# Optimization experiments

Hardware: AMD Instinct MI355X
Metric: run time of the kernel (lower is better)

## Reference

```python
import jax, jax.numpy as jnp
import numpy as np

EPS_Q = 1e-5
EPS_RMS = 1e-6


def _bitlinear(x, w):
    # absmean ternary weight quantization with STE (STE irrelevant for fwd)
    w_scale = jnp.maximum(jnp.mean(jnp.abs(w)), EPS_Q)
    w_q = jnp.clip(jnp.round(w / w_scale), -1.0, 1.0)
    w_q = jax.lax.stop_gradient(w_q - w) + w
    # per-token absmax activation quantization
    x_scale = jnp.maximum(jnp.max(jnp.abs(x), axis=-1, keepdims=True), EPS_Q)
    x_s = x / x_scale
    out = jnp.einsum('bi,oi->bo', x_s, w_q)
    return out * x_scale


def _rmsnorm(x, g):
    rms = jnp.sqrt(jnp.mean(x * x, axis=-1, keepdims=True) + EPS_RMS)
    return x / rms * g


def setup_inputs() -> dict:
    key = jax.random.key(0)
    ks = jax.random.split(key, 6)
    B, IN, H, OUT = 65536, 784, 1024, 10
    return {
        'x': jax.random.normal(ks[0], (B, IN), dtype=jnp.float32),
        'w1': jax.random.normal(ks[1], (H, IN), dtype=jnp.float32) * 0.02,
        'g1': jnp.ones((H,), dtype=jnp.float32),
        'w2': jax.random.normal(ks[2], (H, H), dtype=jnp.float32) * 0.02,
        'g2': jnp.ones((H,), dtype=jnp.float32),
        'w3': jax.random.normal(ks[3], (OUT, H), dtype=jnp.float32) * 0.02,
    }


def reference(x, w1, g1, w2, g2, w3):
    h = _bitlinear(x, w1)
    h = jax.nn.gelu(_rmsnorm(h, g1), approximate=False)
    h = _bitlinear(h, w2)
    h = jax.nn.gelu(_rmsnorm(h, g2), approximate=False)
    return _bitlinear(h, w3)
```

## Files before the change

### kernel.cpp

```cpp
#include <hip/hip_runtime.h>
#include <hip/hip_bf16.h>
#include <stdint.h>


typedef __attribute__((ext_vector_type(8))) short short8;
typedef __attribute__((ext_vector_type(4))) float f32x4;

#define B_TOTAL 65536
#define IN_DIM 784
#define IN_PAD 896
#define H_DIM 1024
#define OUT_DIM 10
#define OUT_PAD 16

__device__ __forceinline__ unsigned short f2bf(float f) {
    union { float f; unsigned u; } c; c.f = f;
    unsigned r = c.u + 0x7FFFu + ((c.u >> 16) & 1u);
    return (unsigned short)(r >> 16);
}
__device__ __forceinline__ float bf2f(unsigned short h) {
    union { unsigned u; float f; } c; c.u = ((unsigned)h) << 16;
    return c.f;
}

__device__ __forceinline__ float gelu_fast(float t) {
    const float z = t * 0.70710678118f;
    const float s = fabsf(z);
    const float tt = 1.0f / (1.0f + 0.3275911f * s);
    const float e = __expf(-s * s);
    float p = fmaf(tt, 1.061405429f, -1.453152027f);
    p = fmaf(tt, p, 1.421413741f);
    p = fmaf(tt, p, -0.284496736f);
    p = fmaf(tt, p, 0.254829592f);
    float erfa = fmaf(-p * tt, e, 1.0f);
    erfa = copysignf(erfa, z);
    return 0.5f * t * (1.0f + erfa);
}

#define GLOAD16(gp, lp)                                                        \
    __builtin_amdgcn_global_load_lds(                                          \
        (const __attribute__((address_space(1))) void*)(gp),                   \
        (__attribute__((address_space(3))) void*)(lp), 16, 0, 0)

__global__ void absum3_kernel(const float* __restrict__ w1, const float* __restrict__ w2,
                              const float* __restrict__ w3, double* acc) {
    __shared__ float red[4];
    const int which = blockIdx.y;
    const float* w = (which == 0) ? w1 : (which == 1) ? w2 : w3;
    const int n = (which == 0) ? H_DIM * IN_DIM : (which == 1) ? H_DIM * H_DIM : OUT_DIM * H_DIM;
    float s = 0.f;
    for (int i = blockIdx.x * blockDim.x + threadIdx.x; i < n; i += gridDim.x * blockDim.x)
        s += fabsf(w[i]);
#pragma unroll
    for (int o = 32; o > 0; o >>= 1) s += __shfl_xor(s, o);
    if ((threadIdx.x & 63) == 0) red[threadIdx.x >> 6] = s;
    __syncthreads();
    if (threadIdx.x == 0) {
        float t = red[0] + red[1] + red[2] + red[3];
        atomicAdd(acc + which, (double)t);
    }
}

__global__ void quant_all(const float* __restrict__ w1, const float* __restrict__ w2,
                          const float* __restrict__ w3,
                          unsigned short* __restrict__ w1q, unsigned short* __restrict__ w2q,
                          unsigned short* __restrict__ w3q, const double* sums) {
    const int k = blockIdx.x * blockDim.x + threadIdx.x;
    const int y = blockIdx.y;
    const float* w; unsigned short* wq; int o, O, K, Kp, n; const double* sum;
    if (y < 1024)      { w = w1; wq = w1q; o = y;        O = H_DIM;  K = IN_DIM; Kp = IN_PAD; n = H_DIM * IN_DIM;  sum = sums + 0; }
    else if (y < 2048) { w = w2; wq = w2q; o = y - 1024; O = H_DIM;  K = H_DIM;  Kp = H_DIM;  n = H_DIM * H_DIM;  sum = sums + 1; }
    else               { w = w3; wq = w3q; o = y - 2048; O = OUT_DIM; K = H_DIM; Kp = H_DIM;  n = OUT_DIM * H_DIM; sum = sums + 2; }
    if (k >= Kp) return;
    float scale = fmaxf((float)(*sum / (double)n), 1e-5f);
    float q = 0.f;
    if (o < O && k < K) {
        float r = rintf(w[(size_t)o * K + k] / scale);
        q = fminf(1.f, fmaxf(-1.f, r));
    }
    wq[(size_t)o * Kp + k] = f2bf(q);
}

__global__ __launch_bounds__(256)
void convert_pad(const float* __restrict__ x, unsigned short* __restrict__ xb) {
    const int g = blockIdx.x * 256 + threadIdx.x;
    const int row = g / 112;
    const int c = (g % 112) * 8;
    short8 v = 0;
    if (c < IN_DIM) {
        const float* p = x + (size_t)row * IN_DIM + c;
        float4 f0 = *(const float4*)p;
        float4 f1 = *(const float4*)(p + 4);
        v[0] = (short)f2bf(f0.x); v[1] = (short)f2bf(f0.y);
        v[2] = (short)f2bf(f0.z); v[3] = (short)f2bf(f0.w);
        v[4] = (short)f2bf(f1.x); v[5] = (short)f2bf(f1.y);
        v[6] = (short)f2bf(f1.z); v[7] = (short)f2bf(f1.w);
    }
    *(short8*)(xb + (size_t)row * IN_PAD + c) = v;
}

template<int KP>
__global__ __launch_bounds__(512, 2)
void gemm_bt(const unsigned short* __restrict__ A, const unsigned short* __restrict__ Bq,
             unsigned short* __restrict__ C) {
    constexpr int NT = KP / 64;
    __shared__ __attribute__((aligned(16))) unsigned short LDS[65536];
    const int tid = threadIdx.x;
    const int lane = tid & 63;
    const int w = tid >> 6;
    const int wm = w >> 2, wn = w & 3;
    const int lr = lane & 15, gq = lane >> 4;
    const int gsw8 = (gq ^ ((lr >> 3) << 1)) * 8;
    const int lrO = lr * 32;
    const int bid = blockIdx.x;
    const int xcd = bid & 7, slot = bid >> 3;
    const int nblk = slot & 3;
    const int mblk = xcd * (gridDim.x >> 5) + (slot >> 2);
    const int m0 = mblk * 256, n0 = nblk * 256;
    const int rS = lane >> 2;
    const int cS = ((lane & 3) ^ ((lane >> 5) << 1)) * 8;
    const int stA0 = w;
    const int stA1 = 8 + w;
    const int stB_P1 = (w >> 2) * 8 + (w & 3);
    const int stB_P3 = stB_P1 + 4;

#define STG(gbase, areaS, st)                                                  \
    {   const unsigned short* _g = (gbase) +                                   \
            (size_t)(((st) >> 1) * 16 + rS) * KP + ((st) & 1) * 32 + cS;       \
        GLOAD16(_g, &LDS[(areaS) + (st) * 512]);                               \
        GLOAD16(_g + (size_t)128 * KP, &LDS[(areaS) + (st) * 512 + 8192]); }
#define ABASE(t) (A + (size_t)m0 * KP + (t) * 64)
#define BBASE(t) (Bq + (size_t)n0 * KP + (t) * 64)
#define LD_A(mq)                                                               \
    _Pragma("unroll") for (int mf = 0; mf < 4; ++mf)                           \
    _Pragma("unroll") for (int kk = 0; kk < 2; ++kk)                           \
        af[mf][kk] = *(const short8*)&LDS[curS +                               \
            ((wm * 8 + (mq) * 4 + mf) * 2 + kk) * 512 + lrO + gsw8];
#define LD_B(nq)                                                               \
    _Pragma("unroll") for (int nf = 0; nf < 2; ++nf)                           \
    _Pragma("unroll") for (int kk = 0; kk < 2; ++kk)                           \
        bf[nf][kk] = *(const short8*)&LDS[curS + 16384 +                       \
            ((wn * 4 + (nq) * 2 + nf) * 2 + kk) * 512 + lrO + gsw8];
#define QMM(mq, nq)                                                            \
    _Pragma("unroll") for (int kk = 0; kk < 2; ++kk)                           \
    _Pragma("unroll") for (int mf = 0; mf < 4; ++mf)                           \
    _Pragma("unroll") for (int nf = 0; nf < 2; ++nf)                           \
        acc[(mq) * 4 + mf][(nq) * 2 + nf] =                                    \
            __builtin_amdgcn_mfma_f32_16x16x32_bf16(af[mf][kk], bf[nf][kk],    \
                acc[(mq) * 4 + mf][(nq) * 2 + nf], 0, 0, 0);

    f32x4 acc[8][4] = {};
    short8 af[4][2], bf[2][2];
    STG(ABASE(0), 0, stA0);
    STG(BBASE(0), 16384, stB_P1);
    STG(BBASE(0), 16384, stB_P3);
    STG(ABASE(0), 0, stA1);
    STG(ABASE(1), 32768, stA0);
    STG(BBASE(1), 49152, stB_P3);
    STG(ABASE(1), 32768, stA1);
    asm volatile("s_waitcnt vmcnt(6)" ::: "memory");
#pragma unroll 2
    for (int t = 0; t < NT; ++t) {
        const int curS = (t & 1) * 32768;
        const int nxtS = curS ^ 32768;
        __builtin_amdgcn_s_barrier();
        LD_A(0); LD_B(0);
        __builtin_amdgcn_s_setprio(1); QMM(0, 0); __builtin_amdgcn_s_setprio(0);
        if (t + 1 < NT) STG(BBASE(t + 1), nxtS + 16384, stB_P1);
        __builtin_amdgcn_s_barrier();
        LD_B(1);
        __builtin_amdgcn_s_setprio(1); QMM(0, 1); __builtin_amdgcn_s_setprio(0);
        if (t + 2 < NT) STG(ABASE(t + 2), curS, stA0);
        __builtin_amdgcn_s_barrier();
        LD_A(1);
        __builtin_amdgcn_s_setprio(1); QMM(1, 1); __builtin_amdgcn_s_setprio(0);
        if (t + 2 < NT) STG(BBASE(t + 2), curS + 16384, stB_P3);
        __builtin_amdgcn_s_barrier();
        LD_B(0);
        __builtin_amdgcn_s_setprio(1); QMM(1, 0); __builtin_amdgcn_s_setprio(0);
        if (t + 2 < NT) STG(ABASE(t + 2), curS, stA1);
        if (t < NT - 2) {
            asm volatile("s_waitcnt vmcnt(6)" ::: "memory");
        } else {
            asm volatile("s_waitcnt vmcnt(0)" ::: "memory");
        }
    }
#pragma unroll
    for (int mf = 0; mf < 8; ++mf) {
        const int grow = m0 + wm * 128 + mf * 16 + (lane >> 4) * 4;
#pragma unroll
        for (int nf = 0; nf < 4; ++nf) {
            const int gcol = n0 + wn * 64 + nf * 16 + lr;
            unsigned short* Cp = C + (size_t)grow * H_DIM + gcol;
#pragma unroll
            for (int j = 0; j < 4; ++j) Cp[(size_t)j * H_DIM] = f2bf(acc[mf][nf][j]);
        }
    }
#undef STG
#undef ABASE
#undef BBASE
#undef LD_A
#undef LD_B
#undef QMM
}

__global__ __launch_bounds__(256)
void norm_gelu(const unsigned short* __restrict__ Hp, const float* __restrict__ g,
               unsigned short* __restrict__ U) {
    const int row = blockIdx.x * 4 + (threadIdx.x >> 6);
    const int lane = threadIdx.x & 63;
    const unsigned short* rp = Hp + (size_t)row * H_DIM;
    short8 v0 = *(const short8*)(rp + lane * 8);
    short8 v1 = *(const short8*)(rp + 512 + lane * 8);
    float f[16];
#pragma unroll
    for (int j = 0; j < 8; ++j) {
        f[j] = bf2f((unsigned short)v0[j]);
        f[8 + j] = bf2f((unsigned short)v1[j]);
    }
    float s = 0.f;
#pragma unroll
    for (int j = 0; j < 16; ++j) s += f[j] * f[j];
#pragma unroll
    for (int o = 32; o > 0; o >>= 1) s += __shfl_xor(s, o);
    const float rinv = 1.f / sqrtf(s * (1.f / 1024.f) + 1e-6f);
    float4 ga0 = *(const float4*)(g + lane * 8);
    float4 ga1 = *(const float4*)(g + lane * 8 + 4);
    float4 gb0 = *(const float4*)(g + 512 + lane * 8);
    float4 gb1 = *(const float4*)(g + 512 + lane * 8 + 4);
    float gv[16] = {ga0.x, ga0.y, ga0.z, ga0.w, ga1.x, ga1.y, ga1.z, ga1.w,
                    gb0.x, gb0.y, gb0.z, gb0.w, gb1.x, gb1.y, gb1.z, gb1.w};
    short8 o0, o1;
#pragma unroll
    for (int j = 0; j < 8; ++j) {
        o0[j] = (short)f2bf(gelu_fast(f[j] * rinv * gv[j]));
        o1[j] = (short)f2bf(gelu_fast(f[8 + j] * rinv * gv[8 + j]));
    }
    unsigned short* up = U + (size_t)row * H_DIM;
    *(short8*)(up + lane * 8) = o0;
    *(short8*)(up + 512 + lane * 8) = o1;
}

__global__ __launch_bounds__(256)
void norm_gelu_out(const unsigned short* __restrict__ Hp, const float* __restrict__ g,
                   const unsigned short* __restrict__ w3q, float* __restrict__ out) {
    __shared__ unsigned short Us[16][1032];
    __shared__ unsigned short Ws[16][1032];
    const int tid = threadIdx.x;
    const int lane = tid & 63, wid = tid >> 6;
    const size_t r0 = (size_t)blockIdx.x * 16;
    for (int i = tid; i < 2048; i += 256) {
        const int r = i >> 7, cg = i & 127;
        *(short8*)&Ws[r][cg * 8] = *(const short8*)(w3q + (size_t)r * H_DIM + cg * 8);
    }
    float4 ga0 = *(const float4*)(g + lane * 8);
    float4 ga1 = *(const float4*)(g + lane * 8 + 4);
    float4 gb0 = *(const float4*)(g + 512 + lane * 8);
    float4 gb1 = *(const float4*)(g + 512 + lane * 8 + 4);
    float gv[16] = {ga0.x, ga0.y, ga0.z, ga0.w, ga1.x, ga1.y, ga1.z, ga1.w,
                    gb0.x, gb0.y, gb0.z, gb0.w, gb1.x, gb1.y, gb1.z, gb1.w};
#pragma unroll
    for (int rr = 0; rr < 4; ++rr) {
        const int row = wid * 4 + rr;
        const unsigned short* rp = Hp + (r0 + row) * H_DIM;
        short8 v0 = *(const short8*)(rp + lane * 8);
        short8 v1 = *(const short8*)(rp + 512 + lane * 8);
        float f[16];
#pragma unroll
        for (int j = 0; j < 8; ++j) {
            f[j] = bf2f((unsigned short)v0[j]);
            f[8 + j] = bf2f((unsigned short)v1[j]);
        }
        float s = 0.f;
#pragma unroll
        for (int j = 0; j < 16; ++j) s += f[j] * f[j];
#pragma unroll
        for (int o = 32; o > 0; o >>= 1) s += __shfl_xor(s, o);
        const float rinv = 1.f / sqrtf(s * (1.f / 1024.f) + 1e-6f);
        short8 o0, o1;
#pragma unroll
        for (int j = 0; j < 8; ++j) {
            o0[j] = (short)f2bf(gelu_fast(f[j] * rinv * gv[j]));
            o1[j] = (short)f2bf(gelu_fast(f[8 + j] * rinv * gv[8 + j]));
        }
        *(short8*)&Us[row][lane * 8] = o0;
        *(short8*)&Us[row][512 + lane * 8] = o1;
    }
    __syncthreads();
    if (wid == 0) {
        const int lr = lane & 15, lk = (lane >> 4) * 8;
        f32x4 acc = {};
#pragma unroll
        for (int ks = 0; ks < 32; ++ks) {
            short8 a = *(const short8*)&Us[lr][ks * 32 + lk];
            short8 b = *(const short8*)&Ws[lr][ks * 32 + lk];
            acc = __builtin_amdgcn_mfma_f32_16x16x32_bf16(a, b, acc, 0, 0, 0);
        }
        if (lr < OUT_DIM) {
#pragma unroll
            for (int j = 0; j < 4; ++j)
                out[(r0 + (lane >> 4) * 4 + j) * OUT_DIM + lr] = acc[j];
        }
    }
}

extern "C" void kernel_launch(void* const* d_in, const int* in_sizes, int n_in,
                              void* d_out, int out_size, void* d_ws, size_t ws_size,
                              hipStream_t stream) {
    (void)in_sizes; (void)n_in; (void)out_size;
    const float* x  = (const float*)d_in[0];
    const float* w1 = (const float*)d_in[1];
    const float* g1 = (const float*)d_in[2];
    const float* w2 = (const float*)d_in[3];
    const float* g2 = (const float*)d_in[4];
    const float* w3 = (const float*)d_in[5];
    float* out = (float*)d_out;

    uint8_t* ws = (uint8_t*)d_ws;
    double* sums = (double*)ws;
    size_t off = 256;
    unsigned short* w1q = (unsigned short*)(ws + off); off += (size_t)H_DIM * IN_PAD * 2;
    unsigned short* w2q = (unsigned short*)(ws + off); off += (size_t)H_DIM * H_DIM * 2;
    unsigned short* w3q = (unsigned short*)(ws + off); off += (size_t)OUT_PAD * H_DIM * 2;

    size_t rem = (ws_size > off) ? ws_size - off : 0;
    int R = B_TOTAL;
    while (R > 2048 && (size_t)2 * R * H_DIM * 2 > rem) R >>= 1;
    unsigned short* bufA = (unsigned short*)(ws + off);
    unsigned short* bufB = bufA + (size_t)R * H_DIM;

    hipMemsetAsync(sums, 0, 3 * sizeof(double), stream);
    absum3_kernel<<<dim3(128, 3), 256, 0, stream>>>(w1, w2, w3, sums);
    quant_all<<<dim3(4, 2064), 256, 0, stream>>>(w1, w2, w3, w1q, w2q, w3q, sums);

    const int nchunk = B_TOTAL / R;
    for (int c = 0; c < nchunk; ++c) {
        const float* xc = x + (size_t)c * R * IN_DIM;
        convert_pad<<<R * 112 / 256, 256, 0, stream>>>(xc, bufB);
        gemm_bt<IN_PAD><<<(R / 256) * 4, 512, 0, stream>>>(bufB, w1q, bufA);
        norm_gelu<<<R / 4, 256, 0, stream>>>(bufA, g1, bufB);
        gemm_bt<H_DIM><<<(R / 256) * 4, 512, 0, stream>>>(bufB, w2q, bufA);
        norm_gelu_out<<<R / 16, 256, 0, stream>>>(bufA, g2, w3q, out + (size_t)c * R * OUT_DIM);
    }
}
```

Before: 463.1 us.

## Restructure GEMM to 4 waves with 128x128 per-wave tiles and simple double buffer

The bf16 GEMM goes from 8 waves per 512-thread block (each wave computing 128x64) to 4 waves per 256-thread block, each computing a 128x128 sub-tile with 64 accumulators. The four-phase interleaved staging schedule with partial vmcnt waits is replaced by a plain double buffer: load all fragments, issue the next tile's global-to-LDS copies, run the MFMAs, then wait for all loads and barrier. This raises register reuse per wave and cuts barriers, but register pressure rises a lot, only one block per CU fits, and global-load latency is less hidden behind compute.

```diff
diff --git a/kernel.cpp b/kernel.cpp
--- a/kernel.cpp
+++ b/kernel.cpp
@@ -100,7 +100,7 @@
 }
 
 template<int KP>
-__global__ __launch_bounds__(512, 2)
+__global__ __launch_bounds__(256, 1)
 void gemm_bt(const unsigned short* __restrict__ A, const unsigned short* __restrict__ Bq,
              unsigned short* __restrict__ C) {
     constexpr int NT = KP / 64;
@@ -108,7 +108,7 @@
     const int tid = threadIdx.x;
     const int lane = tid & 63;
     const int w = tid >> 6;
-    const int wm = w >> 2, wn = w & 3;
+    const int wm = w >> 1, wn = w & 1;
     const int lr = lane & 15, gq = lane >> 4;
     const int gsw8 = (gq ^ ((lr >> 3) << 1)) * 8;
     const int lrO = lr * 32;
@@ -119,89 +119,64 @@
     const int m0 = mblk * 256, n0 = nblk * 256;
     const int rS = lane >> 2;
     const int cS = ((lane & 3) ^ ((lane >> 5) << 1)) * 8;
-    const int stA0 = w;
-    const int stA1 = 8 + w;
-    const int stB_P1 = (w >> 2) * 8 + (w & 3);
-    const int stB_P3 = stB_P1 + 4;
-
-#define STG(gbase, areaS, st)                                                  \
-    {   const unsigned short* _g = (gbase) +                                   \
-            (size_t)(((st) >> 1) * 16 + rS) * KP + ((st) & 1) * 32 + cS;       \
-        GLOAD16(_g, &LDS[(areaS) + (st) * 512]);                               \
-        GLOAD16(_g + (size_t)128 * KP, &LDS[(areaS) + (st) * 512 + 8192]); }
-#define ABASE(t) (A + (size_t)m0 * KP + (t) * 64)
-#define BBASE(t) (Bq + (size_t)n0 * KP + (t) * 64)
-#define LD_A(mq)                                                               \
-    _Pragma("unroll") for (int mf = 0; mf < 4; ++mf)                           \
-    _Pragma("unroll") for (int kk = 0; kk < 2; ++kk)                           \
-        af[mf][kk] = *(const short8*)&LDS[curS +                               \
-            ((wm * 8 + (mq) * 4 + mf) * 2 + kk) * 512 + lrO + gsw8];
-#define LD_B(nq)                                                               \
-    _Pragma("unroll") for (int nf = 0; nf < 2; ++nf)                           \
-    _Pragma("unroll") for (int kk = 0; kk < 2; ++kk)                           \
-        bf[nf][kk] = *(const short8*)&LDS[curS + 16384 +                       \
-            ((wn * 4 + (nq) * 2 + nf) * 2 + kk) * 512 + lrO + gsw8];
-#define QMM(mq, nq)                                                            \
-    _Pragma("unroll") for (int kk = 0; kk < 2; ++kk)                           \
-    _Pragma("unroll") for (int mf = 0; mf < 4; ++mf)                           \
-    _Pragma("unroll") for (int nf = 0; nf < 2; ++nf)                           \
-        acc[(mq) * 4 + mf][(nq) * 2 + nf] =                                    \
-            __builtin_amdgcn_mfma_f32_16x16x32_bf16(af[mf][kk], bf[nf][kk],    \
-                acc[(mq) * 4 + mf][(nq) * 2 + nf], 0, 0, 0);
-
-    f32x4 acc[8][4] = {};
-    short8 af[4][2], bf[2][2];
-    STG(ABASE(0), 0, stA0);
-    STG(BBASE(0), 16384, stB_P1);
-    STG(BBASE(0), 16384, stB_P3);
-    STG(ABASE(0), 0, stA1);
-    STG(ABASE(1), 32768, stA0);
-    STG(BBASE(1), 49152, stB_P3);
-    STG(ABASE(1), 32768, stA1);
-    asm volatile("s_waitcnt vmcnt(6)" ::: "memory");
+
+#define STAGE_TILE(t, bufS)                                                    \
+    _Pragma("unroll") for (int i = 0; i < 8; ++i) {                            \
+        const int st = w * 8 + i;                                              \
+        const int srow = (st >> 1) * 16 + rS;                                  \
+        const int scol = (t) * 64 + (st & 1) * 32 + cS;                        \
+        GLOAD16(A + (size_t)(m0 + srow) * KP + scol, &LDS[(bufS) + st * 512]); \
+        GLOAD16(Bq + (size_t)(n0 + srow) * KP + scol,                          \
+                &LDS[(bufS) + 16384 + st * 512]);                              \
+    }
+
+    f32x4 acc[8][8] = {};
+    short8 af[8][2], bf[8][2];
+    STAGE_TILE(0, 0);
+    asm volatile("s_waitcnt vmcnt(0)" ::: "memory");
+    __builtin_amdgcn_s_barrier();
 #pragma unroll 2
     for (int t = 0; t < NT; ++t) {
-        const int curS = (t & 1) * 32768;
-        const int nxtS = curS ^ 32768;
+        const int bufS = (t & 1) * 32768;
+        const int nxtS = bufS ^ 32768;
+#pragma unroll
+        for (int mf = 0; mf < 8; ++mf)
+            af[mf][0] = *(const short8*)&LDS[bufS + ((wm * 8 + mf) * 2 + 0) * 512 + lrO + gsw8];
+#pragma unroll
+        for (int nf = 0; nf < 8; ++nf)
+            bf[nf][0] = *(const short8*)&LDS[bufS + 16384 + ((wn * 8 + nf) * 2 + 0) * 512 + lrO + gsw8];
+#pragma unroll
+        for (int mf = 0; mf < 8; ++mf)
+            af[mf][1] = *(const short8*)&LDS[bufS + ((wm * 8 + mf) * 2 + 1) * 512 + lrO + gsw8];
+#pragma unroll
+        for (int nf = 0; nf < 8; ++nf)
+            bf[nf][1] = *(const short8*)&LDS[bufS + 16384 + ((wn * 8 + nf) * 2 + 1) * 512 + lrO + gsw8];
+        if (t + 1 < NT) STAGE_TILE(t + 1, nxtS);
+        __builtin_amdgcn_s_setprio(1);
+#pragma unroll
+        for (int kk = 0; kk < 2; ++kk)
+#pragma unroll
+            for (int mf = 0; mf < 8; ++mf)
+#pragma unroll
+                for (int nf = 0; nf < 8; ++nf)
+                    acc[mf][nf] = __builtin_amdgcn_mfma_f32_16x16x32_bf16(
+                        af[mf][kk], bf[nf][kk], acc[mf][nf], 0, 0, 0);
+        __builtin_amdgcn_s_setprio(0);
+        asm volatile("s_waitcnt vmcnt(0)" ::: "memory");
         __builtin_amdgcn_s_barrier();
-        LD_A(0); LD_B(0);
-        __builtin_amdgcn_s_setprio(1); QMM(0, 0); __builtin_amdgcn_s_setprio(0);
-        if (t + 1 < NT) STG(BBASE(t + 1), nxtS + 16384, stB_P1);
-        __builtin_amdgcn_s_barrier();
-        LD_B(1);
-        __builtin_amdgcn_s_setprio(1); QMM(0, 1); __builtin_amdgcn_s_setprio(0);
-        if (t + 2 < NT) STG(ABASE(t + 2), curS, stA0);
-        __builtin_amdgcn_s_barrier();
-        LD_A(1);
-        __builtin_amdgcn_s_setprio(1); QMM(1, 1); __builtin_amdgcn_s_setprio(0);
-        if (t + 2 < NT) STG(BBASE(t + 2), curS + 16384, stB_P3);
-        __builtin_amdgcn_s_barrier();
-        LD_B(0);
-        __builtin_amdgcn_s_setprio(1); QMM(1, 0); __builtin_amdgcn_s_setprio(0);
-        if (t + 2 < NT) STG(ABASE(t + 2), curS, stA1);
-        if (t < NT - 2) {
-            asm volatile("s_waitcnt vmcnt(6)" ::: "memory");
-        } else {
-            asm volatile("s_waitcnt vmcnt(0)" ::: "memory");
-        }
     }
 #pragma unroll
     for (int mf = 0; mf < 8; ++mf) {
         const int grow = m0 + wm * 128 + mf * 16 + (lane >> 4) * 4;
 #pragma unroll
-        for (int nf = 0; nf < 4; ++nf) {
-            const int gcol = n0 + wn * 64 + nf * 16 + lr;
+        for (int nf = 0; nf < 8; ++nf) {
+            const int gcol = n0 + wn * 128 + nf * 16 + lr;
             unsigned short* Cp = C + (size_t)grow * H_DIM + gcol;
 #pragma unroll
             for (int j = 0; j < 4; ++j) Cp[(size_t)j * H_DIM] = f2bf(acc[mf][nf][j]);
         }
     }
-#undef STG
-#undef ABASE
-#undef BBASE
-#undef LD_A
-#undef LD_B
-#undef QMM
+#undef STAGE_TILE
 }
 
 __global__ __launch_bounds__(256)
@@ -337,9 +312,9 @@
     for (int c = 0; c < nchunk; ++c) {
         const float* xc = x + (size_t)c * R * IN_DIM;
         convert_pad<<<R * 112 / 256, 256, 0, stream>>>(xc, bufB);
-        gemm_bt<IN_PAD><<<(R / 256) * 4, 512, 0, stream>>>(bufB, w1q, bufA);
+        gemm_bt<IN_PAD><<<(R / 256) * 4, 256, 0, stream>>>(bufB, w1q, bufA);
         norm_gelu<<<R / 4, 256, 0, stream>>>(bufA, g1, bufB);
-        gemm_bt<H_DIM><<<(R / 256) * 4, 512, 0, stream>>>(bufB, w2q, bufA);
+        gemm_bt<H_DIM><<<(R / 256) * 4, 256, 0, stream>>>(bufB, w2q, bufA);
         norm_gelu_out<<<R / 16, 256, 0, stream>>>(bufA, g2, w3q, out + (size_t)c * R * OUT_DIM);
     }
 }
```

New measurement: 959.4 us. +107.2%, slower.

## Shrink layer-1 K padding and use a ping-pong barrier schedule for layer-1 GEMM

Applied to the files above, without the earlier changes.

The first-layer K padding drops from 896 to 832 (13 K-tiles instead of 14), which cuts MFMA work and bytes staged into LDS for the first GEMM and for the conversion kernel. A new GEMM variant is added for layer 1. It issues the LDS fragment loads and the next global-to-LDS stage before a barrier, waits on lgkmcnt, and fences each MFMA group with barriers, aiming to overlap memory traffic with compute across waves. The extra barriers per K-step add synchronisation cost. The GEMM code is refactored into macros shared by both variants.

```diff
diff --git a/kernel.cpp b/kernel.cpp
--- a/kernel.cpp
+++ b/kernel.cpp
@@ -8,7 +8,7 @@
 
 #define B_TOTAL 65536
 #define IN_DIM 784
-#define IN_PAD 896
+#define IN_PAD 832
 #define H_DIM 1024
 #define OUT_DIM 10
 #define OUT_PAD 16
@@ -84,8 +84,8 @@
 __global__ __launch_bounds__(256)
 void convert_pad(const float* __restrict__ x, unsigned short* __restrict__ xb) {
     const int g = blockIdx.x * 256 + threadIdx.x;
-    const int row = g / 112;
-    const int c = (g % 112) * 8;
+    const int row = g / 104;
+    const int c = (g % 104) * 8;
     short8 v = 0;
     if (c < IN_DIM) {
         const float* p = x + (size_t)row * IN_DIM + c;
@@ -99,38 +99,33 @@
     *(short8*)(xb + (size_t)row * IN_PAD + c) = v;
 }
 
-template<int KP>
-__global__ __launch_bounds__(512, 2)
-void gemm_bt(const unsigned short* __restrict__ A, const unsigned short* __restrict__ Bq,
-             unsigned short* __restrict__ C) {
-    constexpr int NT = KP / 64;
-    __shared__ __attribute__((aligned(16))) unsigned short LDS[65536];
-    const int tid = threadIdx.x;
-    const int lane = tid & 63;
-    const int w = tid >> 6;
-    const int wm = w >> 2, wn = w & 3;
-    const int lr = lane & 15, gq = lane >> 4;
-    const int gsw8 = (gq ^ ((lr >> 3) << 1)) * 8;
-    const int lrO = lr * 32;
-    const int bid = blockIdx.x;
-    const int xcd = bid & 7, slot = bid >> 3;
-    const int nblk = slot & 3;
-    const int mblk = xcd * (gridDim.x >> 5) + (slot >> 2);
-    const int m0 = mblk * 256, n0 = nblk * 256;
-    const int rS = lane >> 2;
-    const int cS = ((lane & 3) ^ ((lane >> 5) << 1)) * 8;
-    const int stA0 = w;
-    const int stA1 = 8 + w;
-    const int stB_P1 = (w >> 2) * 8 + (w & 3);
+#define GEMM_PREAMBLE(KP)                                                      \
+    constexpr int NT = (KP) / 64;                                              \
+    __shared__ __attribute__((aligned(16))) unsigned short LDS[65536];         \
+    const int tid = threadIdx.x;                                               \
+    const int lane = tid & 63;                                                 \
+    const int w = tid >> 6;                                                    \
+    const int wm = w >> 2, wn = w & 3;                                         \
+    const int lr = lane & 15, gq = lane >> 4;                                  \
+    const int gsw8 = (gq ^ ((lr >> 3) << 1)) * 8;                              \
+    const int lrO = lr * 32;                                                   \
+    const int bid = blockIdx.x;                                                \
+    const int xcd = bid & 7, slot = bid >> 3;                                  \
+    const int nblk = slot & 3;                                                 \
+    const int mblk = xcd * (gridDim.x >> 5) + (slot >> 2);                     \
+    const int m0 = mblk * 256, n0 = nblk * 256;                                \
+    const int rS = lane >> 2;                                                  \
+    const int cS = ((lane & 3) ^ ((lane >> 5) << 1)) * 8;                      \
+    const int stA0 = w;                                                        \
+    const int stA1 = 8 + w;                                                    \
+    const int stB_P1 = (w >> 2) * 8 + (w & 3);                                 \
     const int stB_P3 = stB_P1 + 4;
 
-#define STG(gbase, areaS, st)                                                  \
+#define STG(KP, gbase, areaS, st)                                              \
     {   const unsigned short* _g = (gbase) +                                   \
-            (size_t)(((st) >> 1) * 16 + rS) * KP + ((st) & 1) * 32 + cS;       \
+            (size_t)(((st) >> 1) * 16 + rS) * (KP) + ((st) & 1) * 32 + cS;     \
         GLOAD16(_g, &LDS[(areaS) + (st) * 512]);                               \
-        GLOAD16(_g + (size_t)128 * KP, &LDS[(areaS) + (st) * 512 + 8192]); }
-#define ABASE(t) (A + (size_t)m0 * KP + (t) * 64)
-#define BBASE(t) (Bq + (size_t)n0 * KP + (t) * 64)
+        GLOAD16(_g + (size_t)128 * (KP), &LDS[(areaS) + (st) * 512 + 8192]); }
 #define LD_A(mq)                                                               \
     _Pragma("unroll") for (int mf = 0; mf < 4; ++mf)                           \
     _Pragma("unroll") for (int kk = 0; kk < 2; ++kk)                           \
@@ -148,17 +143,34 @@
         acc[(mq) * 4 + mf][(nq) * 2 + nf] =                                    \
             __builtin_amdgcn_mfma_f32_16x16x32_bf16(af[mf][kk], bf[nf][kk],    \
                 acc[(mq) * 4 + mf][(nq) * 2 + nf], 0, 0, 0);
-
+#define GEMM_PROLOGUE(KP)                                                      \
+    STG(KP, A + (size_t)m0 * (KP), 0, stA0);                                   \
+    STG(KP, Bq + (size_t)n0 * (KP), 16384, stB_P1);                            \
+    STG(KP, Bq + (size_t)n0 * (KP), 16384, stB_P3);                            \
+    STG(KP, A + (size_t)m0 * (KP), 0, stA1);                                   \
+    STG(KP, A + (size_t)m0 * (KP) + 64, 32768, stA0);                          \
+    STG(KP, Bq + (size_t)n0 * (KP) + 64, 49152, stB_P3);                       \
+    STG(KP, A + (size_t)m0 * (KP) + 64, 32768, stA1);                          \
+    asm volatile("s_waitcnt vmcnt(6)" ::: "memory");
+#define GEMM_EPILOGUE()                                                        \
+    _Pragma("unroll") for (int mf = 0; mf < 8; ++mf) {                         \
+        const int grow = m0 + wm * 128 + mf * 16 + (lane >> 4) * 4;            \
+        _Pragma("unroll") for (int nf = 0; nf < 4; ++nf) {                     \
+            const int gcol = n0 + wn * 64 + nf * 16 + lr;                      \
+            unsigned short* Cp = C + (size_t)grow * H_DIM + gcol;              \
+            _Pragma("unroll") for (int j = 0; j < 4; ++j)                      \
+                Cp[(size_t)j * H_DIM] = f2bf(acc[mf][nf][j]);                  \
+        }                                                                      \
+    }
+
+template<int KP>
+__global__ __launch_bounds__(512, 2)
+void gemm_bt(const unsigned short* __restrict__ A, const unsigned short* __restrict__ Bq,
+             unsigned short* __restrict__ C) {
+    GEMM_PREAMBLE(KP)
     f32x4 acc[8][4] = {};
     short8 af[4][2], bf[2][2];
-    STG(ABASE(0), 0, stA0);
-    STG(BBASE(0), 16384, stB_P1);
-    STG(BBASE(0), 16384, stB_P3);
-    STG(ABASE(0), 0, stA1);
-    STG(ABASE(1), 32768, stA0);
-    STG(BBASE(1), 49152, stB_P3);
-    STG(ABASE(1), 32768, stA1);
-    asm volatile("s_waitcnt vmcnt(6)" ::: "memory");
+    GEMM_PROLOGUE(KP)
 #pragma unroll 2
     for (int t = 0; t < NT; ++t) {
         const int curS = (t & 1) * 32768;
@@ -166,42 +178,66 @@
         __builtin_amdgcn_s_barrier();
         LD_A(0); LD_B(0);
         __builtin_amdgcn_s_setprio(1); QMM(0, 0); __builtin_amdgcn_s_setprio(0);
-        if (t + 1 < NT) STG(BBASE(t + 1), nxtS + 16384, stB_P1);
+        if (t + 1 < NT) STG(KP, Bq + (size_t)n0 * KP + (t + 1) * 64, nxtS + 16384, stB_P1);
         __builtin_amdgcn_s_barrier();
         LD_B(1);
         __builtin_amdgcn_s_setprio(1); QMM(0, 1); __builtin_amdgcn_s_setprio(0);
-        if (t + 2 < NT) STG(ABASE(t + 2), curS, stA0);
+        if (t + 2 < NT) STG(KP, A + (size_t)m0 * KP + (t + 2) * 64, curS, stA0);
         __builtin_amdgcn_s_barrier();
         LD_A(1);
         __builtin_amdgcn_s_setprio(1); QMM(1, 1); __builtin_amdgcn_s_setprio(0);
-        if (t + 2 < NT) STG(BBASE(t + 2), curS + 16384, stB_P3);
+        if (t + 2 < NT) STG(KP, Bq + (size_t)n0 * KP + (t + 2) * 64, curS + 16384, stB_P3);
         __builtin_amdgcn_s_barrier();
         LD_B(0);
         __builtin_amdgcn_s_setprio(1); QMM(1, 0); __builtin_amdgcn_s_setprio(0);
-        if (t + 2 < NT) STG(ABASE(t + 2), curS, stA1);
-        if (t < NT - 2) {
-            asm volatile("s_waitcnt vmcnt(6)" ::: "memory");
-        } else {
-            asm volatile("s_waitcnt vmcnt(0)" ::: "memory");
-        }
-    }
-#pragma unroll
-    for (int mf = 0; mf < 8; ++mf) {
-        const int grow = m0 + wm * 128 + mf * 16 + (lane >> 4) * 4;
-#pragma unroll
-        for (int nf = 0; nf < 4; ++nf) {
-            const int gcol = n0 + wn * 64 + nf * 16 + lr;
-            unsigned short* Cp = C + (size_t)grow * H_DIM + gcol;
-#pragma unroll
-            for (int j = 0; j < 4; ++j) Cp[(size_t)j * H_DIM] = f2bf(acc[mf][nf][j]);
-        }
-    }
-#undef STG
-#undef ABASE
-#undef BBASE
-#undef LD_A
-#undef LD_B
-#undef QMM
+        if (t + 2 < NT) STG(KP, A + (size_t)m0 * KP + (t + 2) * 64, curS, stA1);
+        if (t < NT - 2) { asm volatile("s_waitcnt vmcnt(6)" ::: "memory"); }
+        else            { asm volatile("s_waitcnt vmcnt(0)" ::: "memory"); }
+    }
+    GEMM_EPILOGUE()
+}
+
+template<int KP>
+__global__ __launch_bounds__(512, 2)
+void gemm_bt_v2(const unsigned short* __restrict__ A, const unsigned short* __restrict__ Bq,
+                unsigned short* __restrict__ C) {
+    GEMM_PREAMBLE(KP)
+    f32x4 acc[8][4] = {};
+    short8 af[4][2], bf[2][2];
+    GEMM_PROLOGUE(KP)
+    __builtin_amdgcn_s_barrier();
+#pragma unroll 2
+    for (int t = 0; t < NT; ++t) {
+        const int curS = (t & 1) * 32768;
+        const int nxtS = curS ^ 32768;
+        LD_A(0); LD_B(0);
+        if (t + 1 < NT) STG(KP, Bq + (size_t)n0 * KP + (t + 1) * 64, nxtS + 16384, stB_P1);
+        __builtin_amdgcn_s_barrier();
+        asm volatile("s_waitcnt lgkmcnt(0)" ::: "memory");
+        __builtin_amdgcn_s_setprio(1); QMM(0, 0); __builtin_amdgcn_s_setprio(0);
+        __builtin_amdgcn_s_barrier();
+        LD_B(1);
+        if (t + 2 < NT) STG(KP, A + (size_t)m0 * KP + (t + 2) * 64, curS, stA0);
+        __builtin_amdgcn_s_barrier();
+        asm volatile("s_waitcnt lgkmcnt(0)" ::: "memory");
+        __builtin_amdgcn_s_setprio(1); QMM(0, 1); __builtin_amdgcn_s_setprio(0);
+        __builtin_amdgcn_s_barrier();
+        LD_A(1);
+        if (t + 2 < NT) STG(KP, Bq + (size_t)n0 * KP + (t + 2) * 64, curS + 16384, stB_P3);
+        __builtin_amdgcn_s_barrier();
+        asm volatile("s_waitcnt lgkmcnt(0)" ::: "memory");
+        __builtin_amdgcn_s_setprio(1); QMM(1, 1); __builtin_amdgcn_s_setprio(0);
+        __builtin_amdgcn_s_barrier();
+        LD_B(0);
+        if (t + 2 < NT) STG(KP, A + (size_t)m0 * KP + (t + 2) * 64, curS, stA1);
+        __builtin_amdgcn_s_barrier();
+        asm volatile("s_waitcnt lgkmcnt(0)" ::: "memory");
+        __builtin_amdgcn_s_setprio(1); QMM(1, 0); __builtin_amdgcn_s_setprio(0);
+        if (t < NT - 2) { asm volatile("s_waitcnt vmcnt(6)" ::: "memory"); }
+        else            { asm volatile("s_waitcnt vmcnt(0)" ::: "memory"); }
+        __builtin_amdgcn_s_barrier();
+    }
+    GEMM_EPILOGUE()
 }
 
 __global__ __launch_bounds__(256)
@@ -336,8 +372,8 @@
     const int nchunk = B_TOTAL / R;
     for (int c = 0; c < nchunk; ++c) {
         const float* xc = x + (size_t)c * R * IN_DIM;
-        convert_pad<<<R * 112 / 256, 256, 0, stream>>>(xc, bufB);
-        gemm_bt<IN_PAD><<<(R / 256) * 4, 512, 0, stream>>>(bufB, w1q, bufA);
+        convert_pad<<<R * 104 / 256, 256, 0, stream>>>(xc, bufB);
+        gemm_bt_v2<IN_PAD><<<(R / 256) * 4, 512, 0, stream>>>(bufB, w1q, bufA);
         norm_gelu<<<R / 4, 256, 0, stream>>>(bufA, g1, bufB);
         gemm_bt<H_DIM><<<(R / 256) * 4, 512, 0, stream>>>(bufB, w2q, bufA);
         norm_gelu_out<<<R / 16, 256, 0, stream>>>(bufA, g2, w3q, out + (size_t)c * R * OUT_DIM);
```

New measurement: 448.0 us. 3.3% less time.

## Interleave LDS fragment reads with MFMAs and trim first-layer K padding

Applied to the files above, without the earlier changes.

The GEMM main loop is rewritten so LDS fragment loads for the next quadrant are issued between the MFMA instructions of the current quadrant, rather than as separate load phases before each block of MFMAs. The aim is to hide LDS latency behind matrix-core work. Separately, the first-layer K padding shrinks from 896 to 832 (13 K-tiles of 64 instead of 14), cutting padded MFMA work and the bytes written by the conversion kernel. The interleaved schedule depends on register reuse of af/bf across barriers and may raise register pressure.

```diff
diff --git a/kernel.cpp b/kernel.cpp
--- a/kernel.cpp
+++ b/kernel.cpp
@@ -8,7 +8,7 @@
 
 #define B_TOTAL 65536
 #define IN_DIM 784
-#define IN_PAD 896
+#define IN_PAD 832
 #define H_DIM 1024
 #define OUT_DIM 10
 #define OUT_PAD 16
@@ -84,8 +84,8 @@
 __global__ __launch_bounds__(256)
 void convert_pad(const float* __restrict__ x, unsigned short* __restrict__ xb) {
     const int g = blockIdx.x * 256 + threadIdx.x;
-    const int row = g / 112;
-    const int c = (g % 112) * 8;
+    const int row = g / 104;
+    const int c = (g % 104) * 8;
     short8 v = 0;
     if (c < IN_DIM) {
         const float* p = x + (size_t)row * IN_DIM + c;
@@ -129,61 +129,89 @@
             (size_t)(((st) >> 1) * 16 + rS) * KP + ((st) & 1) * 32 + cS;       \
         GLOAD16(_g, &LDS[(areaS) + (st) * 512]);                               \
         GLOAD16(_g + (size_t)128 * KP, &LDS[(areaS) + (st) * 512 + 8192]); }
-#define ABASE(t) (A + (size_t)m0 * KP + (t) * 64)
-#define BBASE(t) (Bq + (size_t)n0 * KP + (t) * 64)
-#define LD_A(mq)                                                               \
-    _Pragma("unroll") for (int mf = 0; mf < 4; ++mf)                           \
-    _Pragma("unroll") for (int kk = 0; kk < 2; ++kk)                           \
-        af[mf][kk] = *(const short8*)&LDS[curS +                               \
-            ((wm * 8 + (mq) * 4 + mf) * 2 + kk) * 512 + lrO + gsw8];
-#define LD_B(nq)                                                               \
-    _Pragma("unroll") for (int nf = 0; nf < 2; ++nf)                           \
-    _Pragma("unroll") for (int kk = 0; kk < 2; ++kk)                           \
-        bf[nf][kk] = *(const short8*)&LDS[curS + 16384 +                       \
-            ((wn * 4 + (nq) * 2 + nf) * 2 + kk) * 512 + lrO + gsw8];
-#define QMM(mq, nq)                                                            \
-    _Pragma("unroll") for (int kk = 0; kk < 2; ++kk)                           \
-    _Pragma("unroll") for (int mf = 0; mf < 4; ++mf)                           \
-    _Pragma("unroll") for (int nf = 0; nf < 2; ++nf)                           \
-        acc[(mq) * 4 + mf][(nq) * 2 + nf] =                                    \
-            __builtin_amdgcn_mfma_f32_16x16x32_bf16(af[mf][kk], bf[nf][kk],    \
-                acc[(mq) * 4 + mf][(nq) * 2 + nf], 0, 0, 0);
+#define RD_A(mq, mf, kk)                                                       \
+    (*(const short8*)&LDS[curS + ((wm * 8 + (mq) * 4 + (mf)) * 2 + (kk)) * 512 + lrO + gsw8])
+#define RD_B(nq, nf, kk)                                                       \
+    (*(const short8*)&LDS[curS + 16384 + ((wn * 4 + (nq) * 2 + (nf)) * 2 + (kk)) * 512 + lrO + gsw8])
+#define MM(mq, nq, mf, nf, kk)                                                 \
+    acc[(mq) * 4 + (mf)][(nq) * 2 + (nf)] =                                    \
+        __builtin_amdgcn_mfma_f32_16x16x32_bf16(af[mf][kk], bf[nf][kk],        \
+            acc[(mq) * 4 + (mf)][(nq) * 2 + (nf)], 0, 0, 0)
 
     f32x4 acc[8][4] = {};
     short8 af[4][2], bf[2][2];
-    STG(ABASE(0), 0, stA0);
-    STG(BBASE(0), 16384, stB_P1);
-    STG(BBASE(0), 16384, stB_P3);
-    STG(ABASE(0), 0, stA1);
-    STG(ABASE(1), 32768, stA0);
-    STG(BBASE(1), 49152, stB_P3);
-    STG(ABASE(1), 32768, stA1);
+    STG(A + (size_t)m0 * KP, 0, stA0);
+    STG(Bq + (size_t)n0 * KP, 16384, stB_P1);
+    STG(Bq + (size_t)n0 * KP, 16384, stB_P3);
+    STG(A + (size_t)m0 * KP, 0, stA1);
+    STG(A + (size_t)m0 * KP + 64, 32768, stA0);
+    STG(Bq + (size_t)n0 * KP + 64, 49152, stB_P3);
+    STG(A + (size_t)m0 * KP + 64, 32768, stA1);
     asm volatile("s_waitcnt vmcnt(6)" ::: "memory");
 #pragma unroll 2
     for (int t = 0; t < NT; ++t) {
         const int curS = (t & 1) * 32768;
         const int nxtS = curS ^ 32768;
         __builtin_amdgcn_s_barrier();
-        LD_A(0); LD_B(0);
-        __builtin_amdgcn_s_setprio(1); QMM(0, 0); __builtin_amdgcn_s_setprio(0);
-        if (t + 1 < NT) STG(BBASE(t + 1), nxtS + 16384, stB_P1);
+        af[0][0] = RD_A(0, 0, 0); bf[0][0] = RD_B(0, 0, 0);
+        af[1][0] = RD_A(0, 1, 0); bf[1][0] = RD_B(0, 1, 0);
+        __builtin_amdgcn_s_setprio(1);
+        MM(0, 0, 0, 0, 0); af[2][0] = RD_A(0, 2, 0);
+        MM(0, 0, 0, 1, 0); af[3][0] = RD_A(0, 3, 0);
+        MM(0, 0, 1, 0, 0); af[0][1] = RD_A(0, 0, 1);
+        MM(0, 0, 1, 1, 0); bf[0][1] = RD_B(0, 0, 1);
+        MM(0, 0, 2, 0, 0); af[1][1] = RD_A(0, 1, 1);
+        MM(0, 0, 2, 1, 0); bf[1][1] = RD_B(0, 1, 1);
+        MM(0, 0, 3, 0, 0); af[2][1] = RD_A(0, 2, 1);
+        MM(0, 0, 3, 1, 0); af[3][1] = RD_A(0, 3, 1);
+        MM(0, 0, 0, 0, 1); bf[0][0] = RD_B(1, 0, 0);
+        MM(0, 0, 0, 1, 1); bf[1][0] = RD_B(1, 1, 0);
+        MM(0, 0, 1, 0, 1); MM(0, 0, 1, 1, 1);
+        MM(0, 0, 2, 0, 1); MM(0, 0, 2, 1, 1);
+        MM(0, 0, 3, 0, 1); MM(0, 0, 3, 1, 1);
+        __builtin_amdgcn_s_setprio(0);
+        bf[0][1] = RD_B(1, 0, 1); bf[1][1] = RD_B(1, 1, 1);
+        if (t + 1 < NT) STG(Bq + (size_t)n0 * KP + (t + 1) * 64, nxtS + 16384, stB_P1);
         __builtin_amdgcn_s_barrier();
-        LD_B(1);
-        __builtin_amdgcn_s_setprio(1); QMM(0, 1); __builtin_amdgcn_s_setprio(0);
-        if (t + 2 < NT) STG(ABASE(t + 2), curS, stA0);
+        __builtin_amdgcn_s_setprio(1);
+        MM(0, 1, 0, 0, 0); MM(0, 1, 0, 1, 0); af[0][0] = RD_A(1, 0, 0);
+        MM(0, 1, 1, 0, 0); MM(0, 1, 1, 1, 0); af[1][0] = RD_A(1, 1, 0);
+        MM(0, 1, 2, 0, 0); MM(0, 1, 2, 1, 0); af[2][0] = RD_A(1, 2, 0);
+        MM(0, 1, 3, 0, 0); MM(0, 1, 3, 1, 0); af[3][0] = RD_A(1, 3, 0);
+        MM(0, 1, 0, 0, 1); MM(0, 1, 0, 1, 1); af[0][1] = RD_A(1, 0, 1);
+        MM(0, 1, 1, 0, 1); MM(0, 1, 1, 1, 1); af[1][1] = RD_A(1, 1, 1);
+        MM(0, 1, 2, 0, 1); MM(0, 1, 2, 1, 1); af[2][1] = RD_A(1, 2, 1);
+        MM(0, 1, 3, 0, 1); MM(0, 1, 3, 1, 1); af[3][1] = RD_A(1, 3, 1);
+        __builtin_amdgcn_s_setprio(0);
+        if (t + 2 < NT) STG(A + (size_t)m0 * KP + (t + 2) * 64, curS, stA0);
         __builtin_amdgcn_s_barrier();
-        LD_A(1);
-        __builtin_amdgcn_s_setprio(1); QMM(1, 1); __builtin_amdgcn_s_setprio(0);
-        if (t + 2 < NT) STG(BBASE(t + 2), curS + 16384, stB_P3);
+        __builtin_amdgcn_s_setprio(1);
+        MM(1, 1, 0, 0, 0); MM(1, 1, 0, 1, 0);
+        MM(1, 1, 1, 0, 0); MM(1, 1, 1, 1, 0);
+        MM(1, 1, 2, 0, 0); MM(1, 1, 2, 1, 0);
+        MM(1, 1, 3, 0, 0); MM(1, 1, 3, 1, 0);
+        MM(1, 1, 0, 0, 1); bf[0][0] = RD_B(0, 0, 0);
+        MM(1, 1, 0, 1, 1); bf[1][0] = RD_B(0, 1, 0);
+        MM(1, 1, 1, 0, 1); MM(1, 1, 1, 1, 1);
+        MM(1, 1, 2, 0, 1); MM(1, 1, 2, 1, 1);
+        MM(1, 1, 3, 0, 1); MM(1, 1, 3, 1, 1);
+        __builtin_amdgcn_s_setprio(0);
+        bf[0][1] = RD_B(0, 0, 1); bf[1][1] = RD_B(0, 1, 1);
+        if (t + 2 < NT) STG(Bq + (size_t)n0 * KP + (t + 2) * 64, curS + 16384, stB_P3);
         __builtin_amdgcn_s_barrier();
-        LD_B(0);
-        __builtin_amdgcn_s_setprio(1); QMM(1, 0); __builtin_amdgcn_s_setprio(0);
-        if (t + 2 < NT) STG(ABASE(t + 2), curS, stA1);
-        if (t < NT - 2) {
-            asm volatile("s_waitcnt vmcnt(6)" ::: "memory");
-        } else {
-            asm volatile("s_waitcnt vmcnt(0)" ::: "memory");
-        }
+        __builtin_amdgcn_s_setprio(1);
+        MM(1, 0, 0, 0, 0); MM(1, 0, 0, 1, 0);
+        MM(1, 0, 1, 0, 0); MM(1, 0, 1, 1, 0);
+        MM(1, 0, 2, 0, 0); MM(1, 0, 2, 1, 0);
+        MM(1, 0, 3, 0, 0); MM(1, 0, 3, 1, 0);
+        MM(1, 0, 0, 0, 1); MM(1, 0, 0, 1, 1);
+        MM(1, 0, 1, 0, 1); MM(1, 0, 1, 1, 1);
+        MM(1, 0, 2, 0, 1); MM(1, 0, 2, 1, 1);
+        MM(1, 0, 3, 0, 1); MM(1, 0, 3, 1, 1);
+        __builtin_amdgcn_s_setprio(0);
+        if (t + 2 < NT) STG(A + (size_t)m0 * KP + (t + 2) * 64, curS, stA1);
+        if (t < NT - 2) { asm volatile("s_waitcnt vmcnt(6)" ::: "memory"); }
+        else            { asm volatile("s_waitcnt vmcnt(0)" ::: "memory"); }
     }
 #pragma unroll
     for (int mf = 0; mf < 8; ++mf) {
@@ -197,11 +225,9 @@
         }
     }
 #undef STG
-#undef ABASE
-#undef BBASE
-#undef LD_A
-#undef LD_B
-#undef QMM
+#undef RD_A
+#undef RD_B
+#undef MM
 }
 
 __global__ __launch_bounds__(256)
@@ -336,7 +362,7 @@
     const int nchunk = B_TOTAL / R;
     for (int c = 0; c < nchunk; ++c) {
         const float* xc = x + (size_t)c * R * IN_DIM;
-        convert_pad<<<R * 112 / 256, 256, 0, stream>>>(xc, bufB);
+        convert_pad<<<R * 104 / 256, 256, 0, stream>>>(xc, bufB);
         gemm_bt<IN_PAD><<<(R / 256) * 4, 512, 0, stream>>>(bufB, w1q, bufA);
         norm_gelu<<<R / 4, 256, 0, stream>>>(bufA, g1, bufB);
         gemm_bt<H_DIM><<<(R / 256) * 4, 512, 0, stream>>>(bufB, w2q, bufA);
```

Result: faster. 449.8 us (-2.9%).
